# Kernel tuning notes

Measured on AMD Instinct MI355X. Metric: run time of the kernel, lower is better.

Reference implementation:

```python
import jax, jax.numpy as jnp
import numpy as np

B, C1, C2, N1, N2 = 8, 16, 32, 256, 128


def _masks():
    # static numpy masks, mirroring EquivariantLayer.__init__
    n_max, n_min = max(N1, N2), min(N1, N2)
    k = np.arange(n_max)
    k[k > n_max // 2] -= n_max
    mask = np.abs(k) <= n_min / 2            # |k| <= n_min/2 (both nyquists)
    mask2 = mask[: n_max // 2 + 1].copy()    # taken BEFORE removing neg nyquist
    nyq_pos = k == n_min / 2
    nyq_pos2 = nyq_pos[: n_max // 2 + 1]
    nyq_neg = k == -n_min / 2
    mask[nyq_neg] = False                    # drop negative nyquist row
    return mask, mask2, nyq_pos, nyq_pos2

MASK, MASK2, NYQ_POS, NYQ_POS2 = _masks()


def rot90_kernel(t):
    # 90-deg rotation about grid point [0,0] for periodic kernels:
    # transpose last two dims, keep column 0, reverse remaining columns
    t = jnp.swapaxes(t, -1, -2)
    return jnp.concatenate([t[..., :1], t[..., 1:][..., ::-1]], axis=-1)


def symmetric_kernel(kernel):
    # average over the 8 elements of D4 (rotations + transpose*rotations)
    k1 = kernel
    k2 = rot90_kernel(k1)
    k3 = rot90_kernel(k2)
    k4 = rot90_kernel(k3)
    k5 = jnp.swapaxes(k1, -1, -2)
    k6 = rot90_kernel(k5)
    k7 = rot90_kernel(k6)
    k8 = rot90_kernel(k7)
    return (k1 + k2 + k3 + k4 + k5 + k6 + k7 + k8) / 8.0


def _forward(f, kernel):
    F = jnp.fft.rfft2(f)                                  # [b,c1,N1,N1//2+1]
    # downsample: zero nyquist modes, truncate spectrum, rescale
    F = jnp.where(jnp.asarray(NYQ_POS)[None, None, :, None], 0, F)
    F = jnp.where(jnp.asarray(NYQ_POS2)[None, None, None, :], 0, F)
    F = F[:, :, MASK, :][:, :, :, MASK2] * (N2 / N1) ** 2  # [b,c1,N2,N2//2+1]
    # spectral convolution with D4-symmetrized kernel
    K = jnp.fft.rfft2(symmetric_kernel(kernel))            # [1,c1,c2,N2,N2//2+1]
    conv = jnp.einsum('bcnk,cdnk->bdnk', F, K[0])          # sum over input channels
    return jnp.fft.irfft2(F), jnp.fft.irfft2(conv)


def setup_inputs() -> dict:
    key = jax.random.key(0)
    kf, kk = jax.random.split(key)
    f = jax.random.normal(kf, (B, C1, N1, N1), dtype=jnp.float32)
    eps = 0.1
    kernel = eps * (2.0 * jax.random.uniform(kk, (1, C1, C2, N2, N2), dtype=jnp.float32) - 1.0)
    return {"f": f, "kernel": kernel}


def reference(f, kernel):
    return _forward(f, kernel)
```

## Files before the change

### kernel.cpp

```cpp
#include <hip/hip_runtime.h>

#define PI_F 3.14159265358979f

__device__ __forceinline__ float2 cmul(float2 a, float2 b) {
    return make_float2(a.x * b.x - a.y * b.y, a.x * b.y + a.y * b.x);
}
__device__ __forceinline__ float2 cadd(float2 a, float2 b) { return make_float2(a.x + b.x, a.y + b.y); }
__device__ __forceinline__ float2 csub(float2 a, float2 b) { return make_float2(a.x - b.x, a.y - b.y); }
__device__ __forceinline__ float2 shflx(float2 v, int m) {
    return make_float2(__shfl_xor(v.x, m, 64), __shfl_xor(v.y, m, 64));
}
__device__ __forceinline__ float2 shfli(float2 v, int src) {
    return make_float2(__shfl(v.x, src, 64), __shfl(v.y, src, 64));
}
__device__ __forceinline__ int brev6(int x) { return (int)(__brev((unsigned)x) >> 26); }

template<bool INV>
__device__ __forceinline__ void tw_init(int lane, float2* w, float* sg) {
#pragma unroll
    for (int t = 0; t < 6; ++t) {
        int m = 32 >> t;
        bool up = (lane & m) != 0;
        int pos = lane & (m - 1);
        float ang = (INV ? PI_F : -PI_F) * (float)pos / (float)m;
        float sn, cs;
        __sincosf(ang, &sn, &cs);
        w[t]  = up ? make_float2(cs, sn) : make_float2(1.f, 0.f);
        sg[t] = up ? -1.f : 1.f;
    }
}

__device__ __forceinline__ float2 fft64s(float2 v, const float2* w, const float* sg) {
#pragma unroll
    for (int t = 0; t < 6; ++t) {
        int m = 32 >> t;
        float2 p = shflx(v, m);
        float2 d = make_float2(fmaf(sg[t], v.x, p.x), fmaf(sg[t], v.y, p.y));
        v = cmul(d, w[t]);
    }
    return v;
}

__global__ __launch_bounds__(512) void kfft(const float* __restrict__ kin,
                                            float* __restrict__ kout) {
    __shared__ float2 X[128 * 65];
    int img = blockIdx.x;
    int lane = threadIdx.x & 63, wv = threadIdx.x >> 6;
    float2 w[6]; float sg[6];
    tw_init<false>(lane, w, sg);
    int b6 = brev6(lane);
    float sn, cs;
    __sincosf(-PI_F * (float)lane * (1.0f / 64.0f), &sn, &cs);
    float2 w64 = make_float2(cs, sn);
    __sincosf(-PI_F * (float)b6 * (1.0f / 64.0f), &sn, &cs);
    float2 wub = make_float2(cs, sn);
    const float2* in2 = (const float2*)(kin + (size_t)img * 16384);
    int gm2 = brev6((64 - b6) & 63);
#pragma unroll 2
    for (int rr = 0; rr < 16; ++rr) {
        int r = wv * 16 + rr;
        float2 z = in2[r * 64 + lane];
        z = fft64s(z, w, sg);
        float2 zm = shfli(z, gm2);
        float ar = z.x + zm.x, ai = z.y - zm.y;
        float br = z.x - zm.x, bi = z.y + zm.y;
        float p = wub.x * br - wub.y * bi, q = wub.x * bi + wub.y * br;
        X[r * 65 + b6] = make_float2(0.5f * (ar + q), 0.5f * (ai - p));
    }
    __syncthreads();
    float2 c0[8], c1[8];
#pragma unroll
    for (int cc = 0; cc < 8; ++cc) {
        int k = wv * 8 + cc;
        c0[cc] = X[lane * 65 + k];
        c1[cc] = X[(lane + 64) * 65 + k];
    }
    __syncthreads();
    float* Rr = (float*)X;
#pragma unroll
    for (int cc = 0; cc < 8; ++cc) {
        int k = wv * 8 + cc;
        float2 r0 = c0[cc], r1 = c1[cc];
        float2 t = r0;
        r0 = cadd(t, r1);
        r1 = cmul(csub(t, r1), w64);
        r0 = fft64s(r0, w, sg);
        r1 = fft64s(r1, w, sg);
        Rr[(2 * b6) * 65 + k]     = r0.x;
        Rr[(2 * b6 + 1) * 65 + k] = r1.x;
    }
    __syncthreads();
    float4* ko4 = (float4*)(kout + (size_t)img * 8192);
    for (int i = threadIdx.x; i < 2048; i += 512) {
        int n = i >> 4, k4 = (i & 15) << 2;
        float4 o;
        float* op = (float*)&o;
#pragma unroll
        for (int m = 0; m < 4; ++m) {
            int k = k4 + m;
            float t1 = Rr[n * 65 + k];
            float t2 = Rr[((128 - n) & 127) * 65 + k];
            float t3, t4;
            if (n < 64) {
                t3 = Rr[k * 65 + n];
                t4 = Rr[((128 - k) & 127) * 65 + n];
            } else {
                int c2 = 128 - n; if (c2 > 63) c2 = 63;
                t3 = Rr[((128 - k) & 127) * 65 + c2];
                t4 = Rr[k * 65 + c2];
            }
            op[m] = 0.25f * (t1 + t2 + t3 + t4);
        }
        ko4[i] = o;
    }
}

__global__ __launch_bounds__(256) void rfft256(const float* __restrict__ f,
                                               float2* __restrict__ G) {
    int lane = threadIdx.x & 63, wv = threadIdx.x >> 6;
    int row0 = (blockIdx.x * 4 + wv) * 8;
    float2 w[6]; float sg[6];
    tw_init<false>(lane, w, sg);
    float sn, cs;
    __sincosf(-PI_F * (float)lane * (1.0f / 64.0f), &sn, &cs);
    float2 w64 = make_float2(cs, sn);
    __sincosf(-PI_F * (float)lane * (1.0f / 128.0f), &sn, &cs);
    float2 wu = make_float2(cs, sn);
    int srcK = brev6(lane >> 1);
    int srcM = brev6((64 - ((lane + 1) >> 1)) & 63);
#pragma unroll 2
    for (int rr = 0; rr < 8; ++rr) {
        size_t row = (size_t)(row0 + rr);
        const float2* x = (const float2*)(f + row * 256);
        float2 r0 = x[lane], r1 = x[lane + 64];
        float2 t = r0;
        r0 = cadd(t, r1);
        r1 = cmul(csub(t, r1), w64);
        r0 = fft64s(r0, w, sg);
        r1 = fft64s(r1, w, sg);
        float2 e0 = shfli(r0, srcK), o0 = shfli(r1, srcK);
        float2 zk = (lane & 1) ? o0 : e0;
        float2 e1 = shfli(r0, srcM), o1 = shfli(r1, srcM);
        float2 zm = (lane & 1) ? o1 : e1;
        float ar = zk.x + zm.x, ai = zk.y - zm.y;
        float br = zk.x - zm.x, bi = zk.y + zm.y;
        float p = wu.x * br - wu.y * bi, q = wu.x * bi + wu.y * br;
        G[row * 64 + lane] = make_float2(0.5f * (ar + q), 0.5f * (ai - p));
    }
}

__global__ __launch_bounds__(512) void fcol256(const float2* __restrict__ G,
                                               float2* __restrict__ FH) {
    __shared__ float2 S[256 * 33];
    int img = blockIdx.x >> 1, h = blockIdx.x & 1;
    int lane = threadIdx.x & 63, wv = threadIdx.x >> 6;
    float2 w[6]; float sg[6];
    tw_init<false>(lane, w, sg);
    float sn, cs;
    __sincosf(-PI_F * (float)lane * (1.0f / 64.0f), &sn, &cs);
    float2 w64 = make_float2(cs, sn);
    __sincosf(-PI_F * (float)lane * (1.0f / 128.0f), &sn, &cs);
    float2 w128a = make_float2(cs, sn);
    __sincosf(-PI_F * (float)(lane + 64) * (1.0f / 128.0f), &sn, &cs);
    float2 w128b = make_float2(cs, sn);
    const float2* src = G + (size_t)img * 16384 + h * 32;
    for (int i = threadIdx.x; i < 8192; i += 512) {
        int r = i >> 5, c = i & 31;
        S[r * 33 + c] = src[(size_t)r * 64 + c];
    }
    __syncthreads();
    float2 q0[4], q1[4], q2[4], q3[4];
#pragma unroll
    for (int cc = 0; cc < 4; ++cc) {
        int c = wv * 4 + cc;
        q0[cc] = S[(lane)       * 33 + c];
        q1[cc] = S[(lane +  64) * 33 + c];
        q2[cc] = S[(lane + 128) * 33 + c];
        q3[cc] = S[(lane + 192) * 33 + c];
    }
    __syncthreads();
    int b6 = brev6(lane);
#pragma unroll
    for (int cc = 0; cc < 4; ++cc) {
        int c = wv * 4 + cc;
        float2 r0 = q0[cc], r1 = q1[cc], r2 = q2[cc], r3 = q3[cc], t;
        t = r0; r0 = cadd(t, r2); r2 = cmul(csub(t, r2), w128a);
        t = r1; r1 = cadd(t, r3); r3 = cmul(csub(t, r3), w128b);
        t = r0; r0 = cadd(t, r1); r1 = cmul(csub(t, r1), w64);
        t = r2; r2 = cadd(t, r3); r3 = cmul(csub(t, r3), w64);
        r0 = fft64s(r0, w, sg); r1 = fft64s(r1, w, sg);
        r2 = fft64s(r2, w, sg); r3 = fft64s(r3, w, sg);
        float2 vv[4] = { r0, r2, r1, r3 };
#pragma unroll
        for (int j = 0; j < 4; ++j) {
            int n = 4 * b6 + j;
            int r = (n < 64) ? n : ((n >= 193) ? n - 128 : -1);
            if (r >= 0) S[r * 33 + c] = make_float2(vv[j].x * 0.25f, vv[j].y * 0.25f);
        }
    }
    __syncthreads();
    float2* dst = FH + (size_t)img * 8192 + h * 32;
    for (int i = threadIdx.x; i < 4096; i += 512) {
        int r = i >> 5, c = i & 31;
        float2 v = (r == 64) ? make_float2(0.f, 0.f) : S[r * 33 + c];
        dst[(size_t)r * 64 + c] = v;
    }
}

__global__ __launch_bounds__(512) void einsum_rk(const float2* __restrict__ F,
                                                 const float* __restrict__ K,
                                                 float2* __restrict__ C) {
    __shared__ float2 Ft[128 * 32];
    int nk0 = blockIdx.x * 32;
    int t = threadIdx.x;
    for (int i = t; i < 4096; i += 512) {
        int bc = i >> 5, nl = i & 31;
        Ft[i] = F[(size_t)bc * 8192 + nk0 + nl];
    }
    __syncthreads();
    int nl = t & 31, dg = t >> 5;
    int nk = nk0 + nl;
    float2 acc[2][8] = {};
#pragma unroll
    for (int c = 0; c < 16; ++c) {
        float2 fv[8];
#pragma unroll
        for (int b = 0; b < 8; ++b) fv[b] = Ft[(b * 16 + c) * 32 + nl];
#pragma unroll
        for (int j = 0; j < 2; ++j) {
            int d = j * 16 + dg;
            float kv = K[(size_t)(c * 32 + d) * 8192 + nk];
#pragma unroll
            for (int b = 0; b < 8; ++b) {
                acc[j][b].x = fmaf(fv[b].x, kv, acc[j][b].x);
                acc[j][b].y = fmaf(fv[b].y, kv, acc[j][b].y);
            }
        }
    }
#pragma unroll
    for (int j = 0; j < 2; ++j) {
        int d = j * 16 + dg;
#pragma unroll
        for (int b = 0; b < 8; ++b)
            C[(size_t)(b * 32 + d) * 8192 + nk] = acc[j][b];
    }
}

__global__ __launch_bounds__(512) void ifuse(const float2* __restrict__ FH,
                                             const float2* __restrict__ CV,
                                             float* __restrict__ out) {
    __shared__ float2 S[128 * 65];
    int img = blockIdx.x;
    int lane = threadIdx.x & 63, wv = threadIdx.x >> 6;
    float2 w[6]; float sg[6];
    tw_init<true>(lane, w, sg);
    float sn, cs;
    __sincosf(PI_F * (float)lane * (1.0f / 64.0f), &sn, &cs);
    float2 w64 = make_float2(cs, sn);
    const float2* src = (img < 128) ? (FH + (size_t)img * 8192)
                                    : (CV + (size_t)(img - 128) * 8192);
    float2* dst = (float2*)(out + (size_t)img * 16384);
    for (int i = threadIdx.x; i < 8192; i += 512) {
        int r = i >> 6, c = i & 63;
        S[r * 65 + c] = src[i];
    }
    __syncthreads();
    float2 c0[8], c1[8];
#pragma unroll
    for (int cc = 0; cc < 8; ++cc) {
        int k = wv * 8 + cc;
        c0[cc] = S[lane * 65 + k];
        c1[cc] = S[(lane + 64) * 65 + k];
    }
    __syncthreads();
    int b6 = brev6(lane);
#pragma unroll
    for (int cc = 0; cc < 8; ++cc) {
        int k = wv * 8 + cc;
        float2 r0 = c0[cc], r1 = c1[cc];
        float2 t = r0;
        r0 = cadd(t, r1);
        r1 = cmul(csub(t, r1), w64);
        r0 = fft64s(r0, w, sg);
        r1 = fft64s(r1, w, sg);
        S[(2 * b6) * 65 + k]     = r0;
        S[(2 * b6 + 1) * 65 + k] = r1;
    }
    __syncthreads();
#pragma unroll 2
    for (int rr = 0; rr < 16; ++rr) {
        int m = wv * 16 + rr;
        float2 X = S[m * 65 + lane];
        float2 Xm = shfli(X, (64 - lane) & 63);
        if (lane == 0) Xm = make_float2(0.f, 0.f);
        float er = 0.5f * (X.x + Xm.x), ei = 0.5f * (X.y - Xm.y);
        float br = 0.5f * (X.x - Xm.x), bi = 0.5f * (X.y + Xm.y);
        float orr = w64.x * br - w64.y * bi, oi = w64.x * bi + w64.y * br;
        float2 Z = make_float2(er - oi, ei + orr);
        Z = fft64s(Z, w, sg);
        Z = shfli(Z, b6);
        dst[m * 64 + lane] = make_float2(Z.x * (1.0f / 8192.0f), Z.y * (1.0f / 8192.0f));
    }
}

extern "C" void kernel_launch(void* const* d_in, const int* in_sizes, int n_in,
                              void* d_out, int out_size, void* d_ws, size_t ws_size,
                              hipStream_t stream) {
    const float* f   = (const float*)d_in[0];
    const float* kin = (const float*)d_in[1];
    float* out = (float*)d_out;
    char* ws = (char*)d_ws;

    float2* G    = (float2*)ws;
    float2* CONV = (float2*)ws;
    float2* FHAT = (float2*)(ws + 16777216);
    float*  Kr   = (float*)(ws + 33554432);

    kfft<<<512, 512, 0, stream>>>(kin, Kr);
    rfft256<<<1024, 256, 0, stream>>>(f, G);
    fcol256<<<256, 512, 0, stream>>>(G, FHAT);
    einsum_rk<<<256, 512, 0, stream>>>(FHAT, Kr, CONV);
    ifuse<<<384, 512, 0, stream>>>(FHAT, CONV, out);
}
```

Baseline: 181.7 us.

## Merge independent kernels into multi-role launches and use DPP for small butterflies

The kernel FFT and the column FFT now run as separate block ranges of one launch, and the einsum runs in the same launch as the inverse FFT of the downsampled spectrum. This lets independent stages share the GPU instead of serializing. The column-FFT split goes from halves to quarters of the columns, giving more blocks with a smaller shared tile. Butterfly exchanges at distances 1, 2 and 8 use DPP lane moves instead of ds_swizzle/bpermute shuffles. The cost is one extra launch for the conv inverse FFT, and every merged kernel reserves the largest shared-memory footprint.

Result: faster. 164.7 us (-9.4%).

```diff
diff --git a/kernel.cpp b/kernel.cpp
--- a/kernel.cpp
+++ b/kernel.cpp
@@ -14,6 +14,23 @@
     return make_float2(__shfl(v.x, src, 64), __shfl(v.y, src, 64));
 }
 __device__ __forceinline__ int brev6(int x) { return (int)(__brev((unsigned)x) >> 26); }
+
+template<int CTRL>
+__device__ __forceinline__ float dpp1(float x) {
+    return __builtin_bit_cast(float, __builtin_amdgcn_update_dpp(
+        0, __builtin_bit_cast(int, x), CTRL, 0xF, 0xF, true));
+}
+template<int CTRL>
+__device__ __forceinline__ float2 dppx(float2 v) {
+    return make_float2(dpp1<CTRL>(v.x), dpp1<CTRL>(v.y));
+}
+template<int M>
+__device__ __forceinline__ float2 xorx(float2 v) {
+    if constexpr (M == 1)      return dppx<0xB1>(v);
+    else if constexpr (M == 2) return dppx<0x4E>(v);
+    else if constexpr (M == 8) return dppx<0x128>(v);
+    else                       return shflx(v, M);
+}
 
 template<bool INV>
 __device__ __forceinline__ void tw_init(int lane, float2* w, float* sg) {
@@ -31,20 +48,17 @@
 }
 
 __device__ __forceinline__ float2 fft64s(float2 v, const float2* w, const float* sg) {
-#pragma unroll
-    for (int t = 0; t < 6; ++t) {
-        int m = 32 >> t;
-        float2 p = shflx(v, m);
-        float2 d = make_float2(fmaf(sg[t], v.x, p.x), fmaf(sg[t], v.y, p.y));
-        v = cmul(d, w[t]);
-    }
+#define FFT_STAGE(T, M) { float2 p = xorx<M>(v);                                   \
+        float2 d = make_float2(fmaf(sg[T], v.x, p.x), fmaf(sg[T], v.y, p.y));      \
+        v = cmul(d, w[T]); }
+    FFT_STAGE(0, 32) FFT_STAGE(1, 16) FFT_STAGE(2, 8)
+    FFT_STAGE(3, 4)  FFT_STAGE(4, 2)  FFT_STAGE(5, 1)
+#undef FFT_STAGE
     return v;
 }
 
-__global__ __launch_bounds__(512) void kfft(const float* __restrict__ kin,
-                                            float* __restrict__ kout) {
-    __shared__ float2 X[128 * 65];
-    int img = blockIdx.x;
+__device__ void kfft_body(const float* __restrict__ kin, float* __restrict__ kout,
+                          float2* X, int img) {
     int lane = threadIdx.x & 63, wv = threadIdx.x >> 6;
     float2 w[6]; float sg[6];
     tw_init<false>(lane, w, sg);
@@ -112,6 +126,151 @@
             op[m] = 0.25f * (t1 + t2 + t3 + t4);
         }
         ko4[i] = o;
+    }
+}
+
+__device__ void fcol_body(const float2* __restrict__ G, float2* __restrict__ FH,
+                          float2* S, int bid) {
+    int img = bid >> 2, q = bid & 3;
+    int lane = threadIdx.x & 63, wv = threadIdx.x >> 6;
+    float2 w[6]; float sg[6];
+    tw_init<false>(lane, w, sg);
+    float sn, cs;
+    __sincosf(-PI_F * (float)lane * (1.0f / 64.0f), &sn, &cs);
+    float2 w64 = make_float2(cs, sn);
+    __sincosf(-PI_F * (float)lane * (1.0f / 128.0f), &sn, &cs);
+    float2 w128a = make_float2(cs, sn);
+    __sincosf(-PI_F * (float)(lane + 64) * (1.0f / 128.0f), &sn, &cs);
+    float2 w128b = make_float2(cs, sn);
+    const float2* src = G + (size_t)img * 16384 + q * 16;
+    for (int i = threadIdx.x; i < 4096; i += 512) {
+        int r = i >> 4, c = i & 15;
+        S[r * 17 + c] = src[(size_t)r * 64 + c];
+    }
+    __syncthreads();
+    float2 q0[2], q1[2], q2[2], q3[2];
+#pragma unroll
+    for (int cc = 0; cc < 2; ++cc) {
+        int c = wv * 2 + cc;
+        q0[cc] = S[(lane)       * 17 + c];
+        q1[cc] = S[(lane +  64) * 17 + c];
+        q2[cc] = S[(lane + 128) * 17 + c];
+        q3[cc] = S[(lane + 192) * 17 + c];
+    }
+    __syncthreads();
+    int b6 = brev6(lane);
+#pragma unroll
+    for (int cc = 0; cc < 2; ++cc) {
+        int c = wv * 2 + cc;
+        float2 r0 = q0[cc], r1 = q1[cc], r2 = q2[cc], r3 = q3[cc], t;
+        t = r0; r0 = cadd(t, r2); r2 = cmul(csub(t, r2), w128a);
+        t = r1; r1 = cadd(t, r3); r3 = cmul(csub(t, r3), w128b);
+        t = r0; r0 = cadd(t, r1); r1 = cmul(csub(t, r1), w64);
+        t = r2; r2 = cadd(t, r3); r3 = cmul(csub(t, r3), w64);
+        r0 = fft64s(r0, w, sg); r1 = fft64s(r1, w, sg);
+        r2 = fft64s(r2, w, sg); r3 = fft64s(r3, w, sg);
+        float2 vv[4] = { r0, r2, r1, r3 };
+#pragma unroll
+        for (int j = 0; j < 4; ++j) {
+            int n = 4 * b6 + j;
+            int r = (n < 64) ? n : ((n >= 193) ? n - 128 : -1);
+            if (r >= 0) S[r * 17 + c] = make_float2(vv[j].x * 0.25f, vv[j].y * 0.25f);
+        }
+    }
+    __syncthreads();
+    float2* dst = FH + (size_t)img * 8192 + q * 16;
+    for (int i = threadIdx.x; i < 2048; i += 512) {
+        int r = i >> 4, c = i & 15;
+        float2 v = (r == 64) ? make_float2(0.f, 0.f) : S[r * 17 + c];
+        dst[(size_t)r * 64 + c] = v;
+    }
+}
+
+__device__ void einsum_body(const float2* __restrict__ F, const float* __restrict__ K,
+                            float2* __restrict__ C, float2* Ft, int bid) {
+    int nk0 = bid * 32;
+    int t = threadIdx.x;
+    for (int i = t; i < 4096; i += 512) {
+        int bc = i >> 5, nl = i & 31;
+        Ft[i] = F[(size_t)bc * 8192 + nk0 + nl];
+    }
+    __syncthreads();
+    int nl = t & 31, dg = t >> 5;
+    int nk = nk0 + nl;
+    float2 acc[2][8] = {};
+#pragma unroll
+    for (int c = 0; c < 16; ++c) {
+        float2 fv[8];
+#pragma unroll
+        for (int b = 0; b < 8; ++b) fv[b] = Ft[(b * 16 + c) * 32 + nl];
+#pragma unroll
+        for (int j = 0; j < 2; ++j) {
+            int d = j * 16 + dg;
+            float kv = K[(size_t)(c * 32 + d) * 8192 + nk];
+#pragma unroll
+            for (int b = 0; b < 8; ++b) {
+                acc[j][b].x = fmaf(fv[b].x, kv, acc[j][b].x);
+                acc[j][b].y = fmaf(fv[b].y, kv, acc[j][b].y);
+            }
+        }
+    }
+#pragma unroll
+    for (int j = 0; j < 2; ++j) {
+        int d = j * 16 + dg;
+#pragma unroll
+        for (int b = 0; b < 8; ++b)
+            C[(size_t)(b * 32 + d) * 8192 + nk] = acc[j][b];
+    }
+}
+
+__device__ void ifuse_body(const float2* __restrict__ src, float2* __restrict__ dst,
+                           float2* S) {
+    int lane = threadIdx.x & 63, wv = threadIdx.x >> 6;
+    float2 w[6]; float sg[6];
+    tw_init<true>(lane, w, sg);
+    float sn, cs;
+    __sincosf(PI_F * (float)lane * (1.0f / 64.0f), &sn, &cs);
+    float2 w64 = make_float2(cs, sn);
+    for (int i = threadIdx.x; i < 8192; i += 512) {
+        int r = i >> 6, c = i & 63;
+        S[r * 65 + c] = src[i];
+    }
+    __syncthreads();
+    float2 c0[8], c1[8];
+#pragma unroll
+    for (int cc = 0; cc < 8; ++cc) {
+        int k = wv * 8 + cc;
+        c0[cc] = S[lane * 65 + k];
+        c1[cc] = S[(lane + 64) * 65 + k];
+    }
+    __syncthreads();
+    int b6 = brev6(lane);
+#pragma unroll
+    for (int cc = 0; cc < 8; ++cc) {
+        int k = wv * 8 + cc;
+        float2 r0 = c0[cc], r1 = c1[cc];
+        float2 t = r0;
+        r0 = cadd(t, r1);
+        r1 = cmul(csub(t, r1), w64);
+        r0 = fft64s(r0, w, sg);
+        r1 = fft64s(r1, w, sg);
+        S[(2 * b6) * 65 + k]     = r0;
+        S[(2 * b6 + 1) * 65 + k] = r1;
+    }
+    __syncthreads();
+#pragma unroll 2
+    for (int rr = 0; rr < 16; ++rr) {
+        int m = wv * 16 + rr;
+        float2 X = S[m * 65 + lane];
+        float2 Xm = shfli(X, (64 - lane) & 63);
+        if (lane == 0) Xm = make_float2(0.f, 0.f);
+        float er = 0.5f * (X.x + Xm.x), ei = 0.5f * (X.y - Xm.y);
+        float br = 0.5f * (X.x - Xm.x), bi = 0.5f * (X.y + Xm.y);
+        float orr = w64.x * br - w64.y * bi, oi = w64.x * bi + w64.y * br;
+        float2 Z = make_float2(er - oi, ei + orr);
+        Z = fft64s(Z, w, sg);
+        Z = shfli(Z, b6);
+        dst[m * 64 + lane] = make_float2(Z.x * (1.0f / 8192.0f), Z.y * (1.0f / 8192.0f));
     }
 }
 
@@ -149,158 +308,34 @@
     }
 }
 
-__global__ __launch_bounds__(512) void fcol256(const float2* __restrict__ G,
-                                               float2* __restrict__ FH) {
-    __shared__ float2 S[256 * 33];
-    int img = blockIdx.x >> 1, h = blockIdx.x & 1;
-    int lane = threadIdx.x & 63, wv = threadIdx.x >> 6;
-    float2 w[6]; float sg[6];
-    tw_init<false>(lane, w, sg);
-    float sn, cs;
-    __sincosf(-PI_F * (float)lane * (1.0f / 64.0f), &sn, &cs);
-    float2 w64 = make_float2(cs, sn);
-    __sincosf(-PI_F * (float)lane * (1.0f / 128.0f), &sn, &cs);
-    float2 w128a = make_float2(cs, sn);
-    __sincosf(-PI_F * (float)(lane + 64) * (1.0f / 128.0f), &sn, &cs);
-    float2 w128b = make_float2(cs, sn);
-    const float2* src = G + (size_t)img * 16384 + h * 32;
-    for (int i = threadIdx.x; i < 8192; i += 512) {
-        int r = i >> 5, c = i & 31;
-        S[r * 33 + c] = src[(size_t)r * 64 + c];
-    }
-    __syncthreads();
-    float2 q0[4], q1[4], q2[4], q3[4];
-#pragma unroll
-    for (int cc = 0; cc < 4; ++cc) {
-        int c = wv * 4 + cc;
-        q0[cc] = S[(lane)       * 33 + c];
-        q1[cc] = S[(lane +  64) * 33 + c];
-        q2[cc] = S[(lane + 128) * 33 + c];
-        q3[cc] = S[(lane + 192) * 33 + c];
-    }
-    __syncthreads();
-    int b6 = brev6(lane);
-#pragma unroll
-    for (int cc = 0; cc < 4; ++cc) {
-        int c = wv * 4 + cc;
-        float2 r0 = q0[cc], r1 = q1[cc], r2 = q2[cc], r3 = q3[cc], t;
-        t = r0; r0 = cadd(t, r2); r2 = cmul(csub(t, r2), w128a);
-        t = r1; r1 = cadd(t, r3); r3 = cmul(csub(t, r3), w128b);
-        t = r0; r0 = cadd(t, r1); r1 = cmul(csub(t, r1), w64);
-        t = r2; r2 = cadd(t, r3); r3 = cmul(csub(t, r3), w64);
-        r0 = fft64s(r0, w, sg); r1 = fft64s(r1, w, sg);
-        r2 = fft64s(r2, w, sg); r3 = fft64s(r3, w, sg);
-        float2 vv[4] = { r0, r2, r1, r3 };
-#pragma unroll
-        for (int j = 0; j < 4; ++j) {
-            int n = 4 * b6 + j;
-            int r = (n < 64) ? n : ((n >= 193) ? n - 128 : -1);
-            if (r >= 0) S[r * 33 + c] = make_float2(vv[j].x * 0.25f, vv[j].y * 0.25f);
-        }
-    }
-    __syncthreads();
-    float2* dst = FH + (size_t)img * 8192 + h * 32;
-    for (int i = threadIdx.x; i < 4096; i += 512) {
-        int r = i >> 5, c = i & 31;
-        float2 v = (r == 64) ? make_float2(0.f, 0.f) : S[r * 33 + c];
-        dst[(size_t)r * 64 + c] = v;
-    }
-}
-
-__global__ __launch_bounds__(512) void einsum_rk(const float2* __restrict__ F,
-                                                 const float* __restrict__ K,
-                                                 float2* __restrict__ C) {
-    __shared__ float2 Ft[128 * 32];
-    int nk0 = blockIdx.x * 32;
-    int t = threadIdx.x;
-    for (int i = t; i < 4096; i += 512) {
-        int bc = i >> 5, nl = i & 31;
-        Ft[i] = F[(size_t)bc * 8192 + nk0 + nl];
-    }
-    __syncthreads();
-    int nl = t & 31, dg = t >> 5;
-    int nk = nk0 + nl;
-    float2 acc[2][8] = {};
-#pragma unroll
-    for (int c = 0; c < 16; ++c) {
-        float2 fv[8];
-#pragma unroll
-        for (int b = 0; b < 8; ++b) fv[b] = Ft[(b * 16 + c) * 32 + nl];
-#pragma unroll
-        for (int j = 0; j < 2; ++j) {
-            int d = j * 16 + dg;
-            float kv = K[(size_t)(c * 32 + d) * 8192 + nk];
-#pragma unroll
-            for (int b = 0; b < 8; ++b) {
-                acc[j][b].x = fmaf(fv[b].x, kv, acc[j][b].x);
-                acc[j][b].y = fmaf(fv[b].y, kv, acc[j][b].y);
-            }
-        }
-    }
-#pragma unroll
-    for (int j = 0; j < 2; ++j) {
-        int d = j * 16 + dg;
-#pragma unroll
-        for (int b = 0; b < 8; ++b)
-            C[(size_t)(b * 32 + d) * 8192 + nk] = acc[j][b];
-    }
-}
-
-__global__ __launch_bounds__(512) void ifuse(const float2* __restrict__ FH,
-                                             const float2* __restrict__ CV,
+__global__ __launch_bounds__(512) void mega1(const float* __restrict__ kin,
+                                             float* __restrict__ Kr,
+                                             const float2* __restrict__ G,
+                                             float2* __restrict__ FH) {
+    __shared__ float2 SH[128 * 65];
+    int bid = blockIdx.x;
+    if (bid < 512) kfft_body(kin, Kr, SH, bid);
+    else           fcol_body(G, FH, SH, bid - 512);
+}
+
+__global__ __launch_bounds__(512) void mega2(const float2* __restrict__ FH,
+                                             const float* __restrict__ Kr,
+                                             float2* __restrict__ CONV,
                                              float* __restrict__ out) {
-    __shared__ float2 S[128 * 65];
+    __shared__ float2 SH[128 * 65];
+    int bid = blockIdx.x;
+    if (bid < 256) einsum_body(FH, Kr, CONV, SH, bid);
+    else {
+        int img = bid - 256;
+        ifuse_body(FH + (size_t)img * 8192, (float2*)(out + (size_t)img * 16384), SH);
+    }
+}
+
+__global__ __launch_bounds__(512) void ifuse1(const float2* __restrict__ CV,
+                                              float* __restrict__ out1) {
+    __shared__ float2 SH[128 * 65];
     int img = blockIdx.x;
-    int lane = threadIdx.x & 63, wv = threadIdx.x >> 6;
-    float2 w[6]; float sg[6];
-    tw_init<true>(lane, w, sg);
-    float sn, cs;
-    __sincosf(PI_F * (float)lane * (1.0f / 64.0f), &sn, &cs);
-    float2 w64 = make_float2(cs, sn);
-    const float2* src = (img < 128) ? (FH + (size_t)img * 8192)
-                                    : (CV + (size_t)(img - 128) * 8192);
-    float2* dst = (float2*)(out + (size_t)img * 16384);
-    for (int i = threadIdx.x; i < 8192; i += 512) {
-        int r = i >> 6, c = i & 63;
-        S[r * 65 + c] = src[i];
-    }
-    __syncthreads();
-    float2 c0[8], c1[8];
-#pragma unroll
-    for (int cc = 0; cc < 8; ++cc) {
-        int k = wv * 8 + cc;
-        c0[cc] = S[lane * 65 + k];
-        c1[cc] = S[(lane + 64) * 65 + k];
-    }
-    __syncthreads();
-    int b6 = brev6(lane);
-#pragma unroll
-    for (int cc = 0; cc < 8; ++cc) {
-        int k = wv * 8 + cc;
-        float2 r0 = c0[cc], r1 = c1[cc];
-        float2 t = r0;
-        r0 = cadd(t, r1);
-        r1 = cmul(csub(t, r1), w64);
-        r0 = fft64s(r0, w, sg);
-        r1 = fft64s(r1, w, sg);
-        S[(2 * b6) * 65 + k]     = r0;
-        S[(2 * b6 + 1) * 65 + k] = r1;
-    }
-    __syncthreads();
-#pragma unroll 2
-    for (int rr = 0; rr < 16; ++rr) {
-        int m = wv * 16 + rr;
-        float2 X = S[m * 65 + lane];
-        float2 Xm = shfli(X, (64 - lane) & 63);
-        if (lane == 0) Xm = make_float2(0.f, 0.f);
-        float er = 0.5f * (X.x + Xm.x), ei = 0.5f * (X.y - Xm.y);
-        float br = 0.5f * (X.x - Xm.x), bi = 0.5f * (X.y + Xm.y);
-        float orr = w64.x * br - w64.y * bi, oi = w64.x * bi + w64.y * br;
-        float2 Z = make_float2(er - oi, ei + orr);
-        Z = fft64s(Z, w, sg);
-        Z = shfli(Z, b6);
-        dst[m * 64 + lane] = make_float2(Z.x * (1.0f / 8192.0f), Z.y * (1.0f / 8192.0f));
-    }
+    ifuse_body(CV + (size_t)img * 8192, (float2*)(out1 + (size_t)img * 16384), SH);
 }
 
 extern "C" void kernel_launch(void* const* d_in, const int* in_sizes, int n_in,
@@ -316,9 +351,8 @@
     float2* FHAT = (float2*)(ws + 16777216);
     float*  Kr   = (float*)(ws + 33554432);
 
-    kfft<<<512, 512, 0, stream>>>(kin, Kr);
     rfft256<<<1024, 256, 0, stream>>>(f, G);
-    fcol256<<<256, 512, 0, stream>>>(G, FHAT);
-    einsum_rk<<<256, 512, 0, stream>>>(FHAT, Kr, CONV);
-    ifuse<<<384, 512, 0, stream>>>(FHAT, CONV, out);
-}
+    mega1<<<1024, 512, 0, stream>>>(kin, Kr, G, FHAT);
+    mega2<<<384, 512, 0, stream>>>(FHAT, Kr, CONV, out);
+    ifuse1<<<256, 512, 0, stream>>>(CONV, out + 2097152);
+}
```
